# Kernel tuning notes

Measured on AMD Instinct MI355X. Metric: run time of the kernel, lower is better.

The kernel has to match this reference:

```python
import jax, jax.numpy as jnp
import numpy as np

B, S, QD, VD, H = 32, 2048, 1024, 1024, 1024
NEG = -1e9


def setup_inputs() -> dict:
    key = jax.random.key(0)
    ks = jax.random.split(key, 7)
    query = jax.random.normal(ks[0], (B, QD), dtype=jnp.float32)
    value = jax.random.normal(ks[1], (B, S, VD), dtype=jnp.float32)
    mask = jax.random.randint(ks[2], (B, S), 0, 2).astype(bool)
    # params (Linear weights stored as [in, out] for einsum convenience)
    Wq = jax.random.normal(ks[3], (QD, H), dtype=jnp.float32) / np.sqrt(QD)
    bq = jax.random.normal(ks[4], (H,), dtype=jnp.float32) * 0.01
    Wv = jax.random.normal(ks[5], (VD, H), dtype=jnp.float32) / np.sqrt(VD)
    w = jax.random.normal(ks[6], (H,), dtype=jnp.float32) / np.sqrt(H)
    return {"query": query, "value": value, "mask": mask,
            "Wq": Wq, "bq": bq, "Wv": Wv, "w": w}


def reference(query, value, mask, Wq, bq, Wv, w):
    # q-projection: [B, H]
    hq = query @ Wq + bq
    # v-projection: [B, S, H]
    hv = jnp.einsum('bsv,vh->bsh', value, Wv)
    # additive attention energies: [B, S]
    logits = jnp.einsum('bsh,h->bs', jnp.tanh(hq[:, None, :] + hv), w)
    logits = jnp.where(mask, logits, NEG)
    return jax.nn.softmax(logits, axis=-1)
```

## Files before the change

kernel.cpp:

```cpp
#include <hip/hip_runtime.h>
#include <hip/hip_bf16.h>
#include <hip/hip_fp16.h>

typedef _Float16 f16;
typedef _Float16 f16x8 __attribute__((ext_vector_type(8)));
typedef float f32x16 __attribute__((ext_vector_type(16)));
typedef unsigned int u32;

#define BB 32
#define SS 2048
#define HH 1024
#define KK 1024

#define WS_BP 0
#define WS_HQ (2u*1024u*1024u)
#define WS_LP (WS_HQ + 131072u)

__device__ __forceinline__ float tanh_f(float x) {
    float e = __expf(2.0f * x);
    return 1.0f - 2.0f * __builtin_amdgcn_rcpf(e + 1.0f);
}

__device__ __forceinline__ void write_a16(char* dst, int off, float4 va, float4 vb) {
    union { f16 h[8]; uint4 u; } pk;
    pk.h[0] = (f16)va.x; pk.h[1] = (f16)va.y; pk.h[2] = (f16)va.z; pk.h[3] = (f16)va.w;
    pk.h[4] = (f16)vb.x; pk.h[5] = (f16)vb.y; pk.h[6] = (f16)vb.z; pk.h[7] = (f16)vb.w;
    *(uint4*)(dst + off) = pk.u;
}

__global__ void pack_wv(const float* __restrict__ Wv, f16* __restrict__ BP) {
    int i = blockIdx.x * 256 + threadIdx.x;
    int k = i >> 10, n = i & 1023;
    float v = Wv[i];
    int ntb = n >> 8, wc = (n >> 6) & 3, ntl = (n >> 5) & 1, nl = n & 31;
    int kit = k >> 6, ks = (k >> 4) & 3, lg = (k >> 3) & 1, j = k & 7;
    int lane = lg * 32 + nl;
    BP[((((((ntb * 16 + kit) * 4 + wc) * 4 + ks) * 2 + ntl) * 64 + lane) * 8) + j] = (f16)v;
}

__global__ void hq_kernel(const float* __restrict__ query, const float* __restrict__ Wq,
                          const float* __restrict__ bq, float* __restrict__ hq) {
    int b = blockIdx.y;
    int h = (blockIdx.x & 3) * 256 + threadIdx.x;
    int v0 = (blockIdx.x >> 2) * 256;
    float acc = 0.f;
#pragma unroll 8
    for (int v = 0; v < 256; ++v)
        acc += query[b * 1024 + v0 + v] * Wq[(v0 + v) * 1024 + h];
    if (v0 == 0) acc += bq[h];
    atomicAdd(&hq[b * 1024 + h], acc);
}

__launch_bounds__(256, 3)
__global__ void fused_main(const float* __restrict__ value, const f16* __restrict__ BP,
                           const float* __restrict__ hq, const float* __restrict__ wvec,
                           float* __restrict__ lpart) {
    __shared__ char A0[8192];
    __shared__ char A1[8192];
    __shared__ float part[256];

    int bid = blockIdx.x;
    int tile = (bid & 7) * 512 + (bid >> 3);
    int Mt = tile >> 2, ntb = tile & 3;
    int m0 = Mt << 6;
    int b = m0 >> 11, s0 = m0 & 2047;

    int tid = threadIdx.x;
    int wc = tid >> 6, l = tid & 63;
    int l31 = l & 31, lg = l >> 5;

    int arow = tid >> 2;
    const float* aga = value + (size_t)(m0 + arow) * 1024 + (tid & 3) * 16;
    int aw0 = ((arow >> 5) * 4 + (tid & 3)) * 1024 + ((arow & 31) << 4);
    int aw1 = aw0 + 512;

    const char* bg = (const char*)BP + (size_t)ntb * 524288 + (size_t)wc * 8192
                   + (size_t)l * 16;

    int a_m0 = l * 16;
    int a_m1 = 4096 + l * 16;

    const f32x16 fzero = {};
    f32x16 acc[2][2];
#pragma unroll
    for (int mt = 0; mt < 2; ++mt)
#pragma unroll
        for (int nt = 0; nt < 2; ++nt) acc[mt][nt] = fzero;

    f16x8 bvA[4], bvB[4];
    float4 ar0, ar1, ar2, ar3;

#define COMPUTE_HALF(Ab, BV, kso) do { \
        f16x8 a00 = *(const f16x8*)((Ab) + a_m0 + ((kso) + 0) * 1024); \
        f16x8 a10 = *(const f16x8*)((Ab) + a_m1 + ((kso) + 0) * 1024); \
        f16x8 a01 = *(const f16x8*)((Ab) + a_m0 + ((kso) + 1) * 1024); \
        f16x8 a11 = *(const f16x8*)((Ab) + a_m1 + ((kso) + 1) * 1024); \
        __builtin_amdgcn_s_setprio(1); \
        acc[0][0] = __builtin_amdgcn_mfma_f32_32x32x16_f16(a00, (BV)[0], acc[0][0], 0, 0, 0); \
        acc[0][1] = __builtin_amdgcn_mfma_f32_32x32x16_f16(a00, (BV)[1], acc[0][1], 0, 0, 0); \
        acc[1][0] = __builtin_amdgcn_mfma_f32_32x32x16_f16(a10, (BV)[0], acc[1][0], 0, 0, 0); \
        acc[1][1] = __builtin_amdgcn_mfma_f32_32x32x16_f16(a10, (BV)[1], acc[1][1], 0, 0, 0); \
        acc[0][0] = __builtin_amdgcn_mfma_f32_32x32x16_f16(a01, (BV)[2], acc[0][0], 0, 0, 0); \
        acc[0][1] = __builtin_amdgcn_mfma_f32_32x32x16_f16(a01, (BV)[3], acc[0][1], 0, 0, 0); \
        acc[1][0] = __builtin_amdgcn_mfma_f32_32x32x16_f16(a11, (BV)[2], acc[1][0], 0, 0, 0); \
        acc[1][1] = __builtin_amdgcn_mfma_f32_32x32x16_f16(a11, (BV)[3], acc[1][1], 0, 0, 0); \
        __builtin_amdgcn_s_setprio(0); \
    } while (0)

#define LOADB(BV, e, half) do { \
        const char* bt_ = bg + (size_t)(e) * 32768 + (half) * 4096; \
        (BV)[0] = *(const f16x8*)(bt_); \
        (BV)[1] = *(const f16x8*)(bt_ + 1024); \
        (BV)[2] = *(const f16x8*)(bt_ + 2048); \
        (BV)[3] = *(const f16x8*)(bt_ + 3072); \
    } while (0)

    {
        const float4* ap = (const float4*)aga;
        ar0 = ap[0]; ar1 = ap[1]; ar2 = ap[2]; ar3 = ap[3];
        write_a16(A0, aw0, ar0, ar1);
        write_a16(A0, aw1, ar2, ar3);
        LOADB(bvA, 0, 0);
        LOADB(bvB, 0, 1);
        asm volatile("s_waitcnt lgkmcnt(0)" ::: "memory");
        __builtin_amdgcn_s_barrier();
    }

#pragma unroll 1
    for (int e = 0; e < 16; ++e) {
        char* Ac = (e & 1) ? A1 : A0;
        char* An = (e & 1) ? A0 : A1;
        int en = (e < 15) ? e + 1 : 15;

        const float4* ap = (const float4*)(aga + en * 64);
        ar0 = ap[0]; ar1 = ap[1]; ar2 = ap[2]; ar3 = ap[3];

        COMPUTE_HALF(Ac, bvA, 0);
        LOADB(bvA, en, 0);
        COMPUTE_HALF(Ac, bvB, 2);
        LOADB(bvB, en, 1);

        write_a16(An, aw0, ar0, ar1);
        write_a16(An, aw1, ar2, ar3);
        asm volatile("s_waitcnt lgkmcnt(0)" ::: "memory");
        __builtin_amdgcn_s_barrier();
    }
#undef COMPUTE_HALF
#undef LOADB

    int h0 = ntb * 256 + wc * 64 + l31;
    int h1 = h0 + 32;
    float hq0 = hq[b * 1024 + h0], hq1 = hq[b * 1024 + h1];
    float w0 = wvec[h0], w1 = wvec[h1];

#pragma unroll
    for (int mt = 0; mt < 2; ++mt) {
#pragma unroll
        for (int i = 0; i < 8; ++i) {
            float pa = tanh_f(hq0 + acc[mt][0][2 * i]) * w0
                     + tanh_f(hq1 + acc[mt][1][2 * i]) * w1;
            float pb = tanh_f(hq0 + acc[mt][0][2 * i + 1]) * w0
                     + tanh_f(hq1 + acc[mt][1][2 * i + 1]) * w1;
            float ea = __shfl_xor(pa, 1), eb = __shfl_xor(pb, 1);
            float g = (l & 1) ? (pb + eb) : (pa + ea);
            g += __shfl_xor(g, 2); g += __shfl_xor(g, 4);
            g += __shfl_xor(g, 8); g += __shfl_xor(g, 16);
            if (l31 < 2) {
                int r = 2 * i + (l31 & 1);
                int row = mt * 32 + (r & 3) + ((r >> 2) << 3) + (lg << 2);
                part[wc * 64 + row] = g;
            }
        }
    }
    __syncthreads();
    if (tid < 64) {
        float s = part[tid] + part[64 + tid] + part[128 + tid] + part[192 + tid];
        lpart[((size_t)ntb * 32 + b) * 2048 + s0 + tid] = s;
    }
}

__global__ void softmax_kernel(const float* __restrict__ lp, const int* __restrict__ mask,
                               float* __restrict__ out) {
    __shared__ float redm[16];
    __shared__ float reds[16];
    const int P = 32 * 2048;
    int b = blockIdx.x, t = threadIdx.x;
    int wid = t >> 6, lane = t & 63;
    int i0 = b * 2048 + t, i1 = i0 + 1024;
    float l0 = lp[i0] + lp[P + i0] + lp[2 * P + i0] + lp[3 * P + i0];
    float l1 = lp[i1] + lp[P + i1] + lp[2 * P + i1] + lp[3 * P + i1];
    float a0 = mask[i0] ? l0 : -1e9f;
    float a1 = mask[i1] ? l1 : -1e9f;
    float mx = fmaxf(a0, a1);
#pragma unroll
    for (int off = 1; off < 64; off <<= 1) mx = fmaxf(mx, __shfl_xor(mx, off));
    if (lane == 0) redm[wid] = mx;
    __syncthreads();
    mx = redm[0];
#pragma unroll
    for (int i = 1; i < 16; ++i) mx = fmaxf(mx, redm[i]);
    float e0 = __expf(a0 - mx), e1 = __expf(a1 - mx);
    float s = e0 + e1;
#pragma unroll
    for (int off = 1; off < 64; off <<= 1) s += __shfl_xor(s, off);
    if (lane == 0) reds[wid] = s;
    __syncthreads();
    float tot = 0.f;
#pragma unroll
    for (int i = 0; i < 16; ++i) tot += reds[i];
    float inv = 1.0f / tot;
    out[b * 2048 + t] = e0 * inv;
    out[b * 2048 + 1024 + t] = e1 * inv;
}

extern "C" void kernel_launch(void* const* d_in, const int* in_sizes, int n_in,
                              void* d_out, int out_size, void* d_ws, size_t ws_size,
                              hipStream_t stream) {
    const float* query = (const float*)d_in[0];
    const float* value = (const float*)d_in[1];
    const int*   mask  = (const int*)d_in[2];
    const float* Wq    = (const float*)d_in[3];
    const float* bq    = (const float*)d_in[4];
    const float* Wv    = (const float*)d_in[5];
    const float* wv    = (const float*)d_in[6];

    char* ws = (char*)d_ws;
    f16*   BP    = (f16*)(ws + WS_BP);
    float* hq    = (float*)(ws + WS_HQ);
    float* lpart = (float*)(ws + WS_LP);
    float* out   = (float*)d_out;

    (void)hipMemsetAsync(hq, 0, BB * HH * sizeof(float), stream);
    pack_wv<<<(KK * HH) / 256, 256, 0, stream>>>(Wv, BP);
    hq_kernel<<<dim3(16, BB), 256, 0, stream>>>(query, Wq, bq, hq);
    fused_main<<<4096, 256, 0, stream>>>(value, BP, hq, wv, lpart);
    softmax_kernel<<<BB, 1024, 0, stream>>>(lpart, mask, out);
}
```

Before: 221.2 us.

## Double M tile to 128 rows per block and interleave A-tile staging

Each block now computes a 128x256 output tile instead of 64x256, so every wave holds 4x2 MFMA accumulators. This halves the grid and halves how often each B fragment must be reloaded per unit of work, raising arithmetic intensity. The A-tile global loads and LDS writes are split into two halves interleaved with the two compute halves. In exchange, accumulator register pressure and LDS use double, and launch bounds drop occupancy from 3 to 2 blocks per CU.

```diff
diff --git a/kernel.cpp b/kernel.cpp
--- a/kernel.cpp
+++ b/kernel.cpp
@@ -51,60 +51,64 @@
     atomicAdd(&hq[b * 1024 + h], acc);
 }
 
-__launch_bounds__(256, 3)
+__launch_bounds__(256, 2)
 __global__ void fused_main(const float* __restrict__ value, const f16* __restrict__ BP,
                            const float* __restrict__ hq, const float* __restrict__ wvec,
                            float* __restrict__ lpart) {
-    __shared__ char A0[8192];
-    __shared__ char A1[8192];
-    __shared__ float part[256];
+    __shared__ char A0[16384];
+    __shared__ char A1[16384];
+    __shared__ float part[512];
 
     int bid = blockIdx.x;
-    int tile = (bid & 7) * 512 + (bid >> 3);
+    int tile = (bid & 7) * 256 + (bid >> 3);
     int Mt = tile >> 2, ntb = tile & 3;
-    int m0 = Mt << 6;
+    int m0 = Mt << 7;
     int b = m0 >> 11, s0 = m0 & 2047;
 
     int tid = threadIdx.x;
     int wc = tid >> 6, l = tid & 63;
     int l31 = l & 31, lg = l >> 5;
 
-    int arow = tid >> 2;
-    const float* aga = value + (size_t)(m0 + arow) * 1024 + (tid & 3) * 16;
-    int aw0 = ((arow >> 5) * 4 + (tid & 3)) * 1024 + ((arow & 31) << 4);
-    int aw1 = aw0 + 512;
+    int arow = tid >> 1, h2 = tid & 1;
+    const float* aga = value + (size_t)(m0 + arow) * 1024 + h2 * 32;
+    int aw[4];
+#pragma unroll
+    for (int q2 = 0; q2 < 4; ++q2)
+        aw[q2] = ((arow >> 5) * 4 + h2 * 2 + (q2 >> 1)) * 1024
+               + (((q2 & 1) * 32 + (arow & 31)) << 4);
 
     const char* bg = (const char*)BP + (size_t)ntb * 524288 + (size_t)wc * 8192
                    + (size_t)l * 16;
 
-    int a_m0 = l * 16;
-    int a_m1 = 4096 + l * 16;
+    int a_rd = l * 16;
 
     const f32x16 fzero = {};
-    f32x16 acc[2][2];
-#pragma unroll
-    for (int mt = 0; mt < 2; ++mt)
+    f32x16 acc[4][2];
+#pragma unroll
+    for (int mt = 0; mt < 4; ++mt)
 #pragma unroll
         for (int nt = 0; nt < 2; ++nt) acc[mt][nt] = fzero;
 
     f16x8 bvA[4], bvB[4];
-    float4 ar0, ar1, ar2, ar3;
 
 #define COMPUTE_HALF(Ab, BV, kso) do { \
-        f16x8 a00 = *(const f16x8*)((Ab) + a_m0 + ((kso) + 0) * 1024); \
-        f16x8 a10 = *(const f16x8*)((Ab) + a_m1 + ((kso) + 0) * 1024); \
-        f16x8 a01 = *(const f16x8*)((Ab) + a_m0 + ((kso) + 1) * 1024); \
-        f16x8 a11 = *(const f16x8*)((Ab) + a_m1 + ((kso) + 1) * 1024); \
-        __builtin_amdgcn_s_setprio(1); \
-        acc[0][0] = __builtin_amdgcn_mfma_f32_32x32x16_f16(a00, (BV)[0], acc[0][0], 0, 0, 0); \
-        acc[0][1] = __builtin_amdgcn_mfma_f32_32x32x16_f16(a00, (BV)[1], acc[0][1], 0, 0, 0); \
-        acc[1][0] = __builtin_amdgcn_mfma_f32_32x32x16_f16(a10, (BV)[0], acc[1][0], 0, 0, 0); \
-        acc[1][1] = __builtin_amdgcn_mfma_f32_32x32x16_f16(a10, (BV)[1], acc[1][1], 0, 0, 0); \
-        acc[0][0] = __builtin_amdgcn_mfma_f32_32x32x16_f16(a01, (BV)[2], acc[0][0], 0, 0, 0); \
-        acc[0][1] = __builtin_amdgcn_mfma_f32_32x32x16_f16(a01, (BV)[3], acc[0][1], 0, 0, 0); \
-        acc[1][0] = __builtin_amdgcn_mfma_f32_32x32x16_f16(a11, (BV)[2], acc[1][0], 0, 0, 0); \
-        acc[1][1] = __builtin_amdgcn_mfma_f32_32x32x16_f16(a11, (BV)[3], acc[1][1], 0, 0, 0); \
-        __builtin_amdgcn_s_setprio(0); \
+        _Pragma("unroll") \
+        for (int ksl = 0; ksl < 2; ++ksl) { \
+            f16x8 a0 = *(const f16x8*)((Ab) + 0 * 4096 + ((kso) + ksl) * 1024 + a_rd); \
+            f16x8 a1 = *(const f16x8*)((Ab) + 1 * 4096 + ((kso) + ksl) * 1024 + a_rd); \
+            f16x8 a2 = *(const f16x8*)((Ab) + 2 * 4096 + ((kso) + ksl) * 1024 + a_rd); \
+            f16x8 a3 = *(const f16x8*)((Ab) + 3 * 4096 + ((kso) + ksl) * 1024 + a_rd); \
+            __builtin_amdgcn_s_setprio(1); \
+            acc[0][0] = __builtin_amdgcn_mfma_f32_32x32x16_f16(a0, (BV)[2 * ksl + 0], acc[0][0], 0, 0, 0); \
+            acc[0][1] = __builtin_amdgcn_mfma_f32_32x32x16_f16(a0, (BV)[2 * ksl + 1], acc[0][1], 0, 0, 0); \
+            acc[1][0] = __builtin_amdgcn_mfma_f32_32x32x16_f16(a1, (BV)[2 * ksl + 0], acc[1][0], 0, 0, 0); \
+            acc[1][1] = __builtin_amdgcn_mfma_f32_32x32x16_f16(a1, (BV)[2 * ksl + 1], acc[1][1], 0, 0, 0); \
+            acc[2][0] = __builtin_amdgcn_mfma_f32_32x32x16_f16(a2, (BV)[2 * ksl + 0], acc[2][0], 0, 0, 0); \
+            acc[2][1] = __builtin_amdgcn_mfma_f32_32x32x16_f16(a2, (BV)[2 * ksl + 1], acc[2][1], 0, 0, 0); \
+            acc[3][0] = __builtin_amdgcn_mfma_f32_32x32x16_f16(a3, (BV)[2 * ksl + 0], acc[3][0], 0, 0, 0); \
+            acc[3][1] = __builtin_amdgcn_mfma_f32_32x32x16_f16(a3, (BV)[2 * ksl + 1], acc[3][1], 0, 0, 0); \
+            __builtin_amdgcn_s_setprio(0); \
+        } \
     } while (0)
 
 #define LOADB(BV, e, half) do { \
@@ -117,9 +121,12 @@
 
     {
         const float4* ap = (const float4*)aga;
-        ar0 = ap[0]; ar1 = ap[1]; ar2 = ap[2]; ar3 = ap[3];
-        write_a16(A0, aw0, ar0, ar1);
-        write_a16(A0, aw1, ar2, ar3);
+        float4 p0 = ap[0], p1 = ap[1], p2 = ap[2], p3 = ap[3];
+        write_a16(A0, aw[0], p0, p1);
+        write_a16(A0, aw[1], p2, p3);
+        float4 p4 = ap[4], p5 = ap[5], p6 = ap[6], p7 = ap[7];
+        write_a16(A0, aw[2], p4, p5);
+        write_a16(A0, aw[3], p6, p7);
         LOADB(bvA, 0, 0);
         LOADB(bvB, 0, 1);
         asm volatile("s_waitcnt lgkmcnt(0)" ::: "memory");
@@ -131,17 +138,20 @@
         char* Ac = (e & 1) ? A1 : A0;
         char* An = (e & 1) ? A0 : A1;
         int en = (e < 15) ? e + 1 : 15;
-
         const float4* ap = (const float4*)(aga + en * 64);
-        ar0 = ap[0]; ar1 = ap[1]; ar2 = ap[2]; ar3 = ap[3];
-
+
+        float4 r0 = ap[0], r1 = ap[1], r2 = ap[2], r3 = ap[3];
         COMPUTE_HALF(Ac, bvA, 0);
         LOADB(bvA, en, 0);
+        write_a16(An, aw[0], r0, r1);
+        write_a16(An, aw[1], r2, r3);
+
+        float4 r4 = ap[4], r5 = ap[5], r6 = ap[6], r7 = ap[7];
         COMPUTE_HALF(Ac, bvB, 2);
         LOADB(bvB, en, 1);
-
-        write_a16(An, aw0, ar0, ar1);
-        write_a16(An, aw1, ar2, ar3);
+        write_a16(An, aw[2], r4, r5);
+        write_a16(An, aw[3], r6, r7);
+
         asm volatile("s_waitcnt lgkmcnt(0)" ::: "memory");
         __builtin_amdgcn_s_barrier();
     }
@@ -154,7 +164,7 @@
     float w0 = wvec[h0], w1 = wvec[h1];
 
 #pragma unroll
-    for (int mt = 0; mt < 2; ++mt) {
+    for (int mt = 0; mt < 4; ++mt) {
 #pragma unroll
         for (int i = 0; i < 8; ++i) {
             float pa = tanh_f(hq0 + acc[mt][0][2 * i]) * w0
@@ -168,13 +178,13 @@
             if (l31 < 2) {
                 int r = 2 * i + (l31 & 1);
                 int row = mt * 32 + (r & 3) + ((r >> 2) << 3) + (lg << 2);
-                part[wc * 64 + row] = g;
+                part[wc * 128 + row] = g;
             }
         }
     }
     __syncthreads();
-    if (tid < 64) {
-        float s = part[tid] + part[64 + tid] + part[128 + tid] + part[192 + tid];
+    if (tid < 128) {
+        float s = part[tid] + part[128 + tid] + part[256 + tid] + part[384 + tid];
         lpart[((size_t)ntb * 32 + b) * 2048 + s0 + tid] = s;
     }
 }
@@ -233,6 +243,6 @@
     (void)hipMemsetAsync(hq, 0, BB * HH * sizeof(float), stream);
     pack_wv<<<(KK * HH) / 256, 256, 0, stream>>>(Wv, BP);
     hq_kernel<<<dim3(16, BB), 256, 0, stream>>>(query, Wq, bq, hq);
-    fused_main<<<4096, 256, 0, stream>>>(value, BP, hq, wv, lpart);
+    fused_main<<<2048, 256, 0, stream>>>(value, BP, hq, wv, lpart);
     softmax_kernel<<<BB, 1024, 0, stream>>>(lpart, mask, out);
 }
```

Result: slower. 239.7 us (+8.3%).
